# Performance work log

Hardware: AMD Instinct MI355X
Metric: run time of the kernel (lower is better)

Reference implementation:

```python
import math
import jax, jax.numpy as jnp
import numpy as np

D_MODEL = 512
NHEAD = 8
D_HEAD = D_MODEL // NHEAD
TEMP = 0.8
B, LQ, LK = 16, 512, 1024
NEG = -1.0e9


def setup_inputs() -> dict:
    key = jax.random.key(0)
    ks = jax.random.split(key, 12)
    s = 1.0 / math.sqrt(D_MODEL)
    return {
        "Q_src": jax.random.normal(ks[0], (B, LQ, D_MODEL), jnp.float32),
        "KV_src": jax.random.normal(ks[1], (B, LK, D_MODEL), jnp.float32),
        "key_gate": jax.random.uniform(ks[2], (B, LK), jnp.float32, 1e-3, 1.0),
        "key_padding_mask": jax.random.randint(ks[3], (B, LK), 0, 2, jnp.int32),
        "Wq": jax.random.normal(ks[4], (D_MODEL, D_MODEL), jnp.float32) * s,
        "bq": jnp.zeros((D_MODEL,), jnp.float32),
        "Wk": jax.random.normal(ks[5], (D_MODEL, D_MODEL), jnp.float32) * s,
        "bk": jnp.zeros((D_MODEL,), jnp.float32),
        "Wv": jax.random.normal(ks[6], (D_MODEL, D_MODEL), jnp.float32) * s,
        "bv": jnp.zeros((D_MODEL,), jnp.float32),
        "Wo": jax.random.normal(ks[7], (D_MODEL, D_MODEL), jnp.float32) * s,
        "bo": jnp.zeros((D_MODEL,), jnp.float32),
    }


def reference(Q_src, KV_src, key_gate, key_padding_mask, Wq, bq, Wk, bk, Wv, bv, Wo, bo):
    b, lq, _ = Q_src.shape
    lk = KV_src.shape[1]
    # projections -> [B, H, L, Dh]
    q = (Q_src @ Wq + bq).reshape(b, lq, NHEAD, D_HEAD).transpose(0, 2, 1, 3)
    k = (KV_src @ Wk + bk).reshape(b, lk, NHEAD, D_HEAD).transpose(0, 2, 1, 3)
    v = (KV_src @ Wv + bv).reshape(b, lk, NHEAD, D_HEAD).transpose(0, 2, 1, 3)
    # scores with log-gate bias [B, H, Lq, Lk]
    logits = jnp.einsum("bhqd,bhkd->bhqk", q, k) / math.sqrt(D_HEAD)
    logits = logits + jnp.log(key_gate)[:, None, None, :]
    pad = (key_padding_mask == 0)[:, None, None, :]
    logits = jnp.where(pad, NEG, logits) / TEMP
    attn = jax.nn.softmax(logits, axis=-1)
    ctx = jnp.einsum("bhqk,bhkd->bhqd", attn, v)
    ctx = ctx.transpose(0, 2, 1, 3).reshape(b, lq, D_MODEL)
    return ctx @ Wo + bo
```

## Files before the change

kernel.cpp:

```cpp
#include <hip/hip_runtime.h>
#include <math.h>

typedef __bf16 bf16;
typedef __bf16 bf16x8 __attribute__((ext_vector_type(8)));
typedef __bf16 bf16x4 __attribute__((ext_vector_type(4)));
typedef __bf16 bf16x2 __attribute__((ext_vector_type(2)));
typedef float  f32x4  __attribute__((ext_vector_type(4)));
typedef unsigned int uint;

#define SCQ2 0.22542110f
#define SMREF 16.0f

#define VMC(n) asm volatile("s_waitcnt vmcnt(" #n ")" ::: "memory")
#define BARR do { __builtin_amdgcn_s_barrier(); __builtin_amdgcn_sched_barrier(0); } while (0)

#if __has_builtin(__builtin_amdgcn_exp2f)
#define EXP2F __builtin_amdgcn_exp2f
#else
#define EXP2F exp2f
#endif

__device__ __forceinline__ void gload16(const void* g, void* l) {
  __builtin_amdgcn_global_load_lds((const __attribute__((address_space(1))) void*)g,
                                   (__attribute__((address_space(3))) void*)l, 16, 0, 0);
}

__device__ __forceinline__ uint pk2(float a, float b) {
  bf16x2 t = {(bf16)a, (bf16)b};
  return __builtin_bit_cast(uint, t);
}

union V8 { bf16x8 v; bf16x4 h[2]; uint u[4]; };

__global__ void prep_k(const float* __restrict__ Wq, const float* __restrict__ Wk,
                       const float* __restrict__ Wv, const float* __restrict__ Wo,
                       bf16* __restrict__ Tq, bf16* __restrict__ Tkv, bf16* __restrict__ To,
                       const float* __restrict__ gate, const int* __restrict__ mask,
                       float* __restrict__ gfac,
                       const float* __restrict__ Qs, const float* __restrict__ KVs,
                       bf16* __restrict__ Qsb, bf16* __restrict__ KVb) {
  const int bid = blockIdx.x, tid = threadIdx.x;
  if (bid < 256) {
    const int w = bid >> 6, t = bid & 63;
    const float* W = (w == 0) ? Wq : (w == 1) ? Wk : (w == 2) ? Wv : Wo;
    bf16* T = (w == 0) ? Tq : (w == 3) ? To : Tkv;
    const int ro = (w == 2) ? 512 : 0;
    const int k0 = (t >> 3) * 64, n0 = (t & 7) * 64;
    __shared__ bf16 tl[64][72];
#pragma unroll
    for (int i = 0; i < 16; i++) {
      int s = i * 256 + tid;
      int r = s >> 6, c = s & 63;
      tl[r][c] = (bf16)W[(size_t)(k0 + r) * 512 + n0 + c];
    }
    __syncthreads();
#pragma unroll
    for (int i = 0; i < 16; i++) {
      int s = i * 256 + tid;
      int r = s >> 6, c = s & 63;
      T[(size_t)(ro + n0 + r) * 512 + k0 + c] = tl[c][r];
    }
  } else if (bid < 320) {
    int i = (bid - 256) * 256 + tid;
    gfac[i] = mask[i] ? __expf(1.25f * __logf(gate[i])) : 0.0f;
  } else {
    const float* s;
    bf16* d;
    size_t i;
    if (bid < 2368) { s = Qs; d = Qsb; i = ((size_t)(bid - 320) * 256 + tid) * 8; }
    else            { s = KVs; d = KVb; i = ((size_t)(bid - 2368) * 256 + tid) * 8; }
    f32x4 a = *(const f32x4*)(s + i);
    f32x4 b = *(const f32x4*)(s + i + 4);
    bf16x8 o = {(bf16)a[0], (bf16)a[1], (bf16)a[2], (bf16)a[3],
                (bf16)b[0], (bf16)b[1], (bf16)b[2], (bf16)b[3]};
    *(bf16x8*)(d + i) = o;
  }
}

__global__ __launch_bounds__(512, 2) void gemm_kv8(
    const bf16* __restrict__ A, const bf16* __restrict__ Bt,
    const float* __restrict__ kb, const float* __restrict__ vb,
    const float* __restrict__ gfac, bf16* __restrict__ K_out, bf16* __restrict__ V_out) {
  const int tid = threadIdx.x, w = tid >> 6, l = tid & 63;
  const int lg = l >> 4, lr = l & 15;
  const int bid = (int)(blockIdx.x & 7) * 32 + (int)(blockIdx.x >> 3);
  const int bm = (bid >> 2) * 256;
  const int bn = (bid & 3) * 256;
  const int wm = w >> 2, wn = w & 3;

  __shared__ __align__(16) bf16 AB[2][16384];

  const int lrow = l >> 2;
  const int cs = (l & 3) ^ ((l >> 3) & 3);

  f32x4 acc[8][4];
#pragma unroll
  for (int i = 0; i < 8; i++)
#pragma unroll
    for (int j = 0; j < 4; j++) acc[i][j] = (f32x4){0.f, 0.f, 0.f, 0.f};

  auto stA = [&](int p, int u, int kt) {
    const int rb = (w >> 2) * 128 + u * 64 + (w & 3) * 16;
    gload16(A + (size_t)(bm + rb + lrow) * 512 + kt * 32 + cs * 8, &AB[p][rb * 32]);
  };
  auto stB = [&](int p, int u, int kt) {
    const int rb = (w >> 1) * 64 + u * 32 + (w & 1) * 16;
    gload16(Bt + (size_t)(bn + rb + lrow) * 512 + kt * 32 + cs * 8, &AB[p][8192 + rb * 32]);
  };

  bf16x8 aA[4], bb0[2], bb1[2];
#define RDA(p, mh)                                                                   \
  _Pragma("unroll") for (int m2 = 0; m2 < 4; m2++) {                                 \
    const int row = wm * 128 + (mh) * 64 + m2 * 16 + lr;                             \
    aA[m2] = *(const bf16x8*)(&AB[p][row * 32 + ((lg ^ ((row >> 1) & 3)) * 8)]);     \
  }
#define RDB(p, nh, dst)                                                              \
  _Pragma("unroll") for (int n2 = 0; n2 < 2; n2++) {                                 \
    const int row = wn * 64 + (nh) * 32 + n2 * 16 + lr;                              \
    dst[n2] = *(const bf16x8*)(&AB[p][8192 + row * 32 + ((lg ^ ((row >> 1) & 3)) * 8)]); \
  }
#define MM(mh, nh, bbv)                                                              \
  __builtin_amdgcn_s_setprio(1);                                                     \
  _Pragma("unroll") for (int m2 = 0; m2 < 4; m2++)                                   \
  _Pragma("unroll") for (int n2 = 0; n2 < 2; n2++)                                   \
    acc[(mh) * 4 + m2][(nh) * 2 + n2] =                                              \
        __builtin_amdgcn_mfma_f32_16x16x32_bf16(aA[m2], bbv[n2],                     \
                                                acc[(mh) * 4 + m2][(nh) * 2 + n2], 0, 0, 0); \
  __builtin_amdgcn_s_setprio(0);

  stA(0, 0, 0); stB(0, 0, 0); stA(0, 1, 0); stB(0, 1, 0);
  stA(1, 0, 1); stB(1, 0, 1);
  VMC(4);
  BARR;

  for (int i = 0; i < 8; ++i) {
    const bool last = (i == 7);
    const int k1 = 2 * i + 1, k2 = 2 * i + 2, k3 = 2 * i + 3;
    stA(1, 1, k1); stB(1, 1, k1);
    RDA(0, 0); RDB(0, 0, bb0);
    MM(0, 0, bb0);
    VMC(4); BARR;
    RDB(0, 1, bb1);
    MM(0, 1, bb1);
    BARR;
    if (!last) stA(0, 0, k2);
    RDA(0, 1);
    MM(1, 0, bb0);
    BARR;
    if (!last) stB(0, 0, k2);
    MM(1, 1, bb1);
    if (last) { VMC(2); } else { VMC(4); }
    BARR;
    if (!last) { stA(0, 1, k2); stB(0, 1, k2); }
    RDA(1, 0); RDB(1, 0, bb0);
    MM(0, 0, bb0);
    if (last) { VMC(0); } else { VMC(4); }
    BARR;
    RDB(1, 1, bb1);
    MM(0, 1, bb1);
    BARR;
    if (!last) stA(1, 0, k3);
    RDA(1, 1);
    MM(1, 0, bb0);
    BARR;
    if (!last) stB(1, 0, k3);
    MM(1, 1, bb1);
    VMC(4); BARR;
  }
#undef RDA
#undef RDB
#undef MM

  if (bn < 512) {
#pragma unroll
    for (int mf = 0; mf < 8; mf++) {
#pragma unroll
      for (int nf = 0; nf < 4; nf++) {
        f32x4 c = acc[mf][nf];
        const int n = bn + wn * 64 + nf * 16 + lr;
        const int m0 = bm + wm * 128 + mf * 16 + lg * 4;
        const float bias = kb[n];
#pragma unroll
        for (int r = 0; r < 4; r++) K_out[(size_t)(m0 + r) * 512 + n] = (bf16)(c[r] + bias);
      }
    }
  } else {
#pragma unroll
    for (int mf = 0; mf < 8; mf++) {
#pragma unroll
      for (int nf = 0; nf < 4; nf++) {
        f32x4 c = acc[mf][nf];
        const int n = bn + wn * 64 + nf * 16 + lr;
        const int m0 = bm + wm * 128 + mf * 16 + lg * 4;
        const int nn = n - 512;
        const int hh = nn >> 6, dd = nn & 63;
        const int bb = m0 >> 10, key = m0 & 1023;
        const int u = key & 31;
        const int keyp = (key & ~31) + ((u & 15) >> 2) * 8 + ((u >> 4) & 1) * 4;
        const float bias = vb[nn];
        f32x4 g4 = *(const f32x4*)(gfac + m0);
        bf16x4 w4 = {(bf16)((c[0] + bias) * g4[0]), (bf16)((c[1] + bias) * g4[1]),
                     (bf16)((c[2] + bias) * g4[2]), (bf16)((c[3] + bias) * g4[3])};
        *(bf16x4*)(V_out + ((size_t)((bb * 8 + hh) * 64 + dd)) * 1024 + keyp) = w4;
      }
    }
  }
}

template <int OM, int NT, int CHUNK>
__global__ __launch_bounds__(256, 2) void gemm_k(
    const bf16* __restrict__ A, const bf16* __restrict__ Bt,
    const float* __restrict__ b0, void* __restrict__ C0, float scale) {
  const int tid = threadIdx.x, w = tid >> 6, l = tid & 63;
  const int lg = l >> 4, lr = l & 15;
  const int bid = (int)(blockIdx.x & 7) * CHUNK + (int)(blockIdx.x >> 3);
  const int bm = (bid / NT) * 64;
  const int bn = (bid % NT) * 128;
  const int wr = (w >> 1) * 32, wc = (w & 1) * 64;
  __shared__ __align__(16) bf16 As[3][64][32];
  __shared__ __align__(16) bf16 Bs[3][128][32];
  const int r16 = l >> 2;
  const int cs = (l & 3) ^ ((l >> 3) & 3);

  f32x4 acc[2][4];
#pragma unroll
  for (int i = 0; i < 2; i++)
#pragma unroll
    for (int j = 0; j < 4; j++) acc[i][j] = (f32x4){0.f, 0.f, 0.f, 0.f};

  auto stage = [&](int buf, int kt) {
    gload16(A + (size_t)(bm + w * 16 + r16) * 512 + kt * 32 + cs * 8, &As[buf][w * 16][0]);
#pragma unroll
    for (int j = 0; j < 2; j++)
      gload16(Bt + (size_t)(bn + w * 32 + j * 16 + r16) * 512 + kt * 32 + cs * 8,
              &Bs[buf][w * 32 + j * 16][0]);
  };

  stage(0, 0);
  stage(1, 1);
  for (int t = 0; t < 16; ++t) {
    const int buf = t % 3;
    if (t == 15) { VMC(0); } else { VMC(3); }
    BARR;
    if (t < 14) stage((t + 2) % 3, t + 2);
    bf16x8 af[2], bfr[4];
#pragma unroll
    for (int mf = 0; mf < 2; mf++) {
      const int row = wr + mf * 16 + lr;
      af[mf] = *(const bf16x8*)(&As[buf][row][(lg ^ ((row >> 1) & 3)) * 8]);
    }
#pragma unroll
    for (int nf = 0; nf < 4; nf++) {
      const int row = wc + nf * 16 + lr;
      bfr[nf] = *(const bf16x8*)(&Bs[buf][row][(lg ^ ((row >> 1) & 3)) * 8]);
    }
    __builtin_amdgcn_s_setprio(1);
#pragma unroll
    for (int mf = 0; mf < 2; mf++)
#pragma unroll
      for (int nf = 0; nf < 4; nf++)
        acc[mf][nf] = __builtin_amdgcn_mfma_f32_16x16x32_bf16(af[mf], bfr[nf], acc[mf][nf], 0, 0, 0);
    __builtin_amdgcn_s_setprio(0);
  }

#pragma unroll
  for (int mf = 0; mf < 2; mf++) {
#pragma unroll
    for (int nf = 0; nf < 4; nf++) {
      f32x4 c = acc[mf][nf];
      const int n = bn + wc + nf * 16 + lr;
      const int m0 = bm + wr + mf * 16 + lg * 4;
      const float bias = b0[n];
      if constexpr (OM == 0) {
        bf16* C = (bf16*)C0;
#pragma unroll
        for (int r = 0; r < 4; r++) C[(size_t)(m0 + r) * 512 + n] = (bf16)((c[r] + bias) * scale);
      } else {
        float* C = (float*)C0;
#pragma unroll
        for (int r = 0; r < 4; r++) C[(size_t)(m0 + r) * 512 + n] = c[r] + bias;
      }
    }
  }
}

__global__ __launch_bounds__(512, 1) void attn_k(
    const bf16* __restrict__ Q, const bf16* __restrict__ Kb,
    const bf16* __restrict__ Vt, const float* __restrict__ gfac,
    bf16* __restrict__ ctx) {
  const int tid = threadIdx.x, w = tid >> 6, l = tid & 63;
  const int lg = l >> 4, lr = l & 15;
  const int bid = (int)(blockIdx.x & 7) * 32 + (int)(blockIdx.x >> 3);
  const int qb = bid & 1, h = (bid >> 1) & 7, b = bid >> 4;
  const int q0 = qb * 256;

  __shared__ __align__(16) bf16 Ks[2][2][64][64];
  __shared__ __align__(16) bf16 Vs[2][2][64][64];
  __shared__ __align__(16) float gfs[1024];

  bf16x8 qf[2][2];
#pragma unroll
  for (int s = 0; s < 2; s++) {
    const bf16* qp = Q + (size_t)(b * 512 + q0 + w * 32 + s * 16 + lr) * 512 + h * 64;
    qf[s][0] = *(const bf16x8*)(qp + lg * 8);
    qf[s][1] = *(const bf16x8*)(qp + 32 + lg * 8);
  }

  f32x4 o[2][4];
#pragma unroll
  for (int s = 0; s < 2; s++)
#pragma unroll
    for (int i = 0; i < 4; i++) o[s][i] = (f32x4){0.f, 0.f, 0.f, 0.f};
  f32x4 lacc[2] = {(f32x4){0.f, 0.f, 0.f, 0.f}, (f32x4){0.f, 0.f, 0.f, 0.f}};

  const int r8 = l >> 3;
  const int c8g = (l & 7) ^ ((l >> 3) & 7);
  const bf16* Kbase = Kb + ((size_t)b * 1024) * 512 + h * 64 + c8g * 8;
  const bf16* Vbase = Vt + ((size_t)(b * 8 + h) * 64) * 1024 + c8g * 8;

  auto stage = [&](int buf, int t) {
#pragma unroll
    for (int sub = 0; sub < 2; sub++) {
      const int kv0 = t * 128 + sub * 64;
      gload16(Kbase + (size_t)(kv0 + w * 8 + r8) * 512, &Ks[buf][sub][w * 8][0]);
      gload16(Vbase + (size_t)(w * 8 + r8) * 1024 + kv0, &Vs[buf][sub][w * 8][0]);
    }
  };

  if (w < 4) gload16(gfac + b * 1024 + w * 256 + l * 4, &gfs[w * 256]);
  stage(0, 0);
  VMC(0);
  BARR;

  for (int t = 0; t < 8; ++t) {
    const int buf = t & 1;
    if (t < 7) stage(buf ^ 1, t + 1);

#pragma unroll
    for (int sub = 0; sub < 2; sub++) {
      f32x4 gvv[4];
#pragma unroll
      for (int f = 0; f < 4; f++)
        gvv[f] = *(const f32x4*)(&gfs[t * 128 + sub * 64 + f * 16 + lg * 4]);

      f32x4 s4[2][4];
      __builtin_amdgcn_s_setprio(1);
#pragma unroll
      for (int f = 0; f < 4; f++) {
        const int row = f * 16 + lr;
        const bf16x8 k0 = *(const bf16x8*)(&Ks[buf][sub][row][(lg ^ (row & 7)) * 8]);
        const bf16x8 k1 = *(const bf16x8*)(&Ks[buf][sub][row][((4 + lg) ^ (row & 7)) * 8]);
#pragma unroll
        for (int s = 0; s < 2; s++) {
          f32x4 z = (f32x4){-SMREF, -SMREF, -SMREF, -SMREF};
          z = __builtin_amdgcn_mfma_f32_16x16x32_bf16(k0, qf[s][0], z, 0, 0, 0);
          s4[s][f] = __builtin_amdgcn_mfma_f32_16x16x32_bf16(k1, qf[s][1], z, 0, 0, 0);
        }
      }
      __builtin_amdgcn_s_setprio(0);

      V8 pb[2][2];
#pragma unroll
      for (int s = 0; s < 2; s++) {
        float p[4][4];
#pragma unroll
        for (int f = 0; f < 4; f++)
#pragma unroll
          for (int r = 0; r < 4; r++) p[f][r] = EXP2F(s4[s][f][r]);
#pragma unroll
        for (int f = 0; f < 4; f++)
#pragma unroll
          for (int r = 0; r < 4; r++) lacc[s][r] = fmaf(p[f][r], gvv[f][r], lacc[s][r]);
        pb[s][0].u[0] = pk2(p[0][0], p[0][1]); pb[s][0].u[1] = pk2(p[0][2], p[0][3]);
        pb[s][0].u[2] = pk2(p[1][0], p[1][1]); pb[s][0].u[3] = pk2(p[1][2], p[1][3]);
        pb[s][1].u[0] = pk2(p[2][0], p[2][1]); pb[s][1].u[1] = pk2(p[2][2], p[2][3]);
        pb[s][1].u[2] = pk2(p[3][0], p[3][1]); pb[s][1].u[3] = pk2(p[3][2], p[3][3]);
      }

      __builtin_amdgcn_s_setprio(1);
#pragma unroll
      for (int od = 0; od < 4; od++) {
        const int row = od * 16 + lr;
        const bf16x8 va0 = *(const bf16x8*)(&Vs[buf][sub][row][(lg ^ (row & 7)) * 8]);
        const bf16x8 va1 = *(const bf16x8*)(&Vs[buf][sub][row][((4 + lg) ^ (row & 7)) * 8]);
#pragma unroll
        for (int s = 0; s < 2; s++) {
          o[s][od] = __builtin_amdgcn_mfma_f32_16x16x32_bf16(va0, pb[s][0].v, o[s][od], 0, 0, 0);
          o[s][od] = __builtin_amdgcn_mfma_f32_16x16x32_bf16(va1, pb[s][1].v, o[s][od], 0, 0, 0);
        }
      }
      __builtin_amdgcn_s_setprio(0);
    }

    if (t < 7) VMC(0);
    BARR;
  }

#pragma unroll
  for (int s = 0; s < 2; s++) {
    float lp = (lacc[s][0] + lacc[s][1]) + (lacc[s][2] + lacc[s][3]);
    lp += __shfl_xor(lp, 16);
    lp += __shfl_xor(lp, 32);
    const float inv = 1.0f / lp;
    bf16* cp = ctx + (size_t)(b * 512 + q0 + w * 32 + s * 16 + lr) * 512 + h * 64;
#pragma unroll
    for (int od = 0; od < 4; od++)
#pragma unroll
      for (int r = 0; r < 4; r++) cp[od * 16 + lg * 4 + r] = (bf16)(o[s][od][r] * inv);
  }
}

extern "C" void kernel_launch(void* const* d_in, const int* in_sizes, int n_in,
                              void* d_out, int out_size, void* d_ws, size_t ws_size,
                              hipStream_t stream) {
  (void)in_sizes; (void)n_in; (void)out_size; (void)ws_size;
  const float* Q_src = (const float*)d_in[0];
  const float* KV_src = (const float*)d_in[1];
  const float* gate = (const float*)d_in[2];
  const int* mask = (const int*)d_in[3];
  const float* Wq = (const float*)d_in[4];
  const float* bq = (const float*)d_in[5];
  const float* Wk = (const float*)d_in[6];
  const float* bk = (const float*)d_in[7];
  const float* Wv = (const float*)d_in[8];
  const float* bv = (const float*)d_in[9];
  const float* Wo = (const float*)d_in[10];
  const float* bo = (const float*)d_in[11];
  float* out = (float*)d_out;

  char* ws = (char*)d_ws;
  size_t off = 0;
  auto alloc = [&](size_t bytes) {
    char* p = ws + off;
    off += (bytes + 255) & ~(size_t)255;
    return p;
  };
  bf16* Wtq = (bf16*)alloc(512 * 512 * 2);
  bf16* Btkv = (bf16*)alloc(1024 * 512 * 2);
  bf16* Wto = (bf16*)alloc(512 * 512 * 2);
  float* gfac = (float*)alloc(16384 * 4);
  bf16* Qsb = (bf16*)alloc((size_t)8192 * 512 * 2);
  bf16* KVb = (bf16*)alloc((size_t)16384 * 512 * 2);
  bf16* Qb = (bf16*)alloc((size_t)8192 * 512 * 2);
  bf16* Kb = (bf16*)alloc((size_t)16384 * 512 * 2);
  bf16* Vt = (bf16*)alloc((size_t)16384 * 512 * 2);
  bf16* Cx = KVb;

  prep_k<<<6464, 256, 0, stream>>>(Wq, Wk, Wv, Wo, Wtq, Btkv, Wto, gate, mask, gfac,
                                   Q_src, KV_src, Qsb, KVb);
  gemm_kv8<<<256, 512, 0, stream>>>(KVb, Btkv, bk, bv, gfac, Kb, Vt);
  gemm_k<0, 4, 64><<<512, 256, 0, stream>>>(Qsb, Wtq, bq, Qb, SCQ2);
  attn_k<<<256, 512, 0, stream>>>(Qb, Kb, Vt, gfac, Cx);
  gemm_k<2, 4, 64><<<512, 256, 0, stream>>>(Cx, Wto, bo, out, 1.0f);
}
```

Baseline: 84.94 us.

## Split KV range across two wave groups with 64-row Q tiles per wave

Restructures the attention kernel so the 8 waves form two groups that each process half of the key/value sequence, with each wave owning 64 query rows instead of 32. K fragments are loaded from LDS once per tile and reused across four query sub-tiles, which cuts LDS read traffic per MFMA. The two groups' partial outputs and row sums are combined through shared memory at the end. This raises register pressure (twice the accumulators and Q fragments) and adds a final reduction and extra barriers.

After: 86.19 us. No clear change (+1.5%).

```diff
diff --git a/kernel.cpp b/kernel.cpp
--- a/kernel.cpp
+++ b/kernel.cpp
@@ -290,6 +290,7 @@
     bf16* __restrict__ ctx) {
   const int tid = threadIdx.x, w = tid >> 6, l = tid & 63;
   const int lg = l >> 4, lr = l & 15;
+  const int ks = w >> 2, wl = w & 3;
   const int bid = (int)(blockIdx.x & 7) * 32 + (int)(blockIdx.x >> 3);
   const int qb = bid & 1, h = (bid >> 1) & 7, b = bid >> 4;
   const int q0 = qb * 256;
@@ -298,20 +299,21 @@
   __shared__ __align__(16) bf16 Vs[2][2][64][64];
   __shared__ __align__(16) float gfs[1024];
 
-  bf16x8 qf[2][2];
-#pragma unroll
-  for (int s = 0; s < 2; s++) {
-    const bf16* qp = Q + (size_t)(b * 512 + q0 + w * 32 + s * 16 + lr) * 512 + h * 64;
+  bf16x8 qf[4][2];
+#pragma unroll
+  for (int s = 0; s < 4; s++) {
+    const bf16* qp = Q + (size_t)(b * 512 + q0 + wl * 64 + s * 16 + lr) * 512 + h * 64;
     qf[s][0] = *(const bf16x8*)(qp + lg * 8);
     qf[s][1] = *(const bf16x8*)(qp + 32 + lg * 8);
   }
 
-  f32x4 o[2][4];
-#pragma unroll
-  for (int s = 0; s < 2; s++)
+  f32x4 o[4][4];
+#pragma unroll
+  for (int s = 0; s < 4; s++)
 #pragma unroll
     for (int i = 0; i < 4; i++) o[s][i] = (f32x4){0.f, 0.f, 0.f, 0.f};
-  f32x4 lacc[2] = {(f32x4){0.f, 0.f, 0.f, 0.f}, (f32x4){0.f, 0.f, 0.f, 0.f}};
+  f32x4 lacc[4] = {(f32x4){0.f, 0.f, 0.f, 0.f}, (f32x4){0.f, 0.f, 0.f, 0.f},
+                   (f32x4){0.f, 0.f, 0.f, 0.f}, (f32x4){0.f, 0.f, 0.f, 0.f}};
 
   const int r8 = l >> 3;
   const int c8g = (l & 7) ^ ((l >> 3) & 7);
@@ -319,94 +321,119 @@
   const bf16* Vbase = Vt + ((size_t)(b * 8 + h) * 64) * 1024 + c8g * 8;
 
   auto stage = [&](int buf, int t) {
-#pragma unroll
-    for (int sub = 0; sub < 2; sub++) {
-      const int kv0 = t * 128 + sub * 64;
-      gload16(Kbase + (size_t)(kv0 + w * 8 + r8) * 512, &Ks[buf][sub][w * 8][0]);
-      gload16(Vbase + (size_t)(w * 8 + r8) * 1024 + kv0, &Vs[buf][sub][w * 8][0]);
-    }
+    const int kv0 = ks * 512 + t * 64;
+    gload16(Kbase + (size_t)(kv0 + wl * 16 + r8) * 512, &Ks[ks][buf][wl * 16][0]);
+    gload16(Kbase + (size_t)(kv0 + wl * 16 + 8 + r8) * 512, &Ks[ks][buf][wl * 16 + 8][0]);
+    gload16(Vbase + (size_t)(wl * 16 + r8) * 1024 + kv0, &Vs[ks][buf][wl * 16][0]);
+    gload16(Vbase + (size_t)(wl * 16 + 8 + r8) * 1024 + kv0, &Vs[ks][buf][wl * 16 + 8][0]);
   };
 
   if (w < 4) gload16(gfac + b * 1024 + w * 256 + l * 4, &gfs[w * 256]);
   stage(0, 0);
-  VMC(0);
-  BARR;
 
   for (int t = 0; t < 8; ++t) {
     const int buf = t & 1;
+    VMC(0);
+    BARR;
     if (t < 7) stage(buf ^ 1, t + 1);
 
-#pragma unroll
-    for (int sub = 0; sub < 2; sub++) {
-      f32x4 gvv[4];
-#pragma unroll
-      for (int f = 0; f < 4; f++)
-        gvv[f] = *(const f32x4*)(&gfs[t * 128 + sub * 64 + f * 16 + lg * 4]);
-
-      f32x4 s4[2][4];
+    f32x4 gvv[4];
+#pragma unroll
+    for (int f = 0; f < 4; f++)
+      gvv[f] = *(const f32x4*)(&gfs[ks * 512 + t * 64 + f * 16 + lg * 4]);
+
+    bf16x8 kf[4][2];
+#pragma unroll
+    for (int f = 0; f < 4; f++) {
+      const int row = f * 16 + lr;
+      kf[f][0] = *(const bf16x8*)(&Ks[ks][buf][row][(lg ^ (row & 7)) * 8]);
+      kf[f][1] = *(const bf16x8*)(&Ks[ks][buf][row][((4 + lg) ^ (row & 7)) * 8]);
+    }
+
+    V8 pb[4][2];
+#pragma unroll
+    for (int s = 0; s < 4; s++) {
+      f32x4 s4[4];
       __builtin_amdgcn_s_setprio(1);
 #pragma unroll
       for (int f = 0; f < 4; f++) {
-        const int row = f * 16 + lr;
-        const bf16x8 k0 = *(const bf16x8*)(&Ks[buf][sub][row][(lg ^ (row & 7)) * 8]);
-        const bf16x8 k1 = *(const bf16x8*)(&Ks[buf][sub][row][((4 + lg) ^ (row & 7)) * 8]);
-#pragma unroll
-        for (int s = 0; s < 2; s++) {
-          f32x4 z = (f32x4){-SMREF, -SMREF, -SMREF, -SMREF};
-          z = __builtin_amdgcn_mfma_f32_16x16x32_bf16(k0, qf[s][0], z, 0, 0, 0);
-          s4[s][f] = __builtin_amdgcn_mfma_f32_16x16x32_bf16(k1, qf[s][1], z, 0, 0, 0);
-        }
+        f32x4 z = (f32x4){-SMREF, -SMREF, -SMREF, -SMREF};
+        z = __builtin_amdgcn_mfma_f32_16x16x32_bf16(kf[f][0], qf[s][0], z, 0, 0, 0);
+        s4[f] = __builtin_amdgcn_mfma_f32_16x16x32_bf16(kf[f][1], qf[s][1], z, 0, 0, 0);
       }
       __builtin_amdgcn_s_setprio(0);
-
-      V8 pb[2][2];
-#pragma unroll
-      for (int s = 0; s < 2; s++) {
-        float p[4][4];
-#pragma unroll
-        for (int f = 0; f < 4; f++)
-#pragma unroll
-          for (int r = 0; r < 4; r++) p[f][r] = EXP2F(s4[s][f][r]);
-#pragma unroll
-        for (int f = 0; f < 4; f++)
-#pragma unroll
-          for (int r = 0; r < 4; r++) lacc[s][r] = fmaf(p[f][r], gvv[f][r], lacc[s][r]);
-        pb[s][0].u[0] = pk2(p[0][0], p[0][1]); pb[s][0].u[1] = pk2(p[0][2], p[0][3]);
-        pb[s][0].u[2] = pk2(p[1][0], p[1][1]); pb[s][0].u[3] = pk2(p[1][2], p[1][3]);
-        pb[s][1].u[0] = pk2(p[2][0], p[2][1]); pb[s][1].u[1] = pk2(p[2][2], p[2][3]);
-        pb[s][1].u[2] = pk2(p[3][0], p[3][1]); pb[s][1].u[3] = pk2(p[3][2], p[3][3]);
+      float p[4][4];
+#pragma unroll
+      for (int f = 0; f < 4; f++)
+#pragma unroll
+        for (int r = 0; r < 4; r++) p[f][r] = EXP2F(s4[f][r]);
+#pragma unroll
+      for (int f = 0; f < 4; f++)
+#pragma unroll
+        for (int r = 0; r < 4; r++) lacc[s][r] = fmaf(p[f][r], gvv[f][r], lacc[s][r]);
+      pb[s][0].u[0] = pk2(p[0][0], p[0][1]); pb[s][0].u[1] = pk2(p[0][2], p[0][3]);
+      pb[s][0].u[2] = pk2(p[1][0], p[1][1]); pb[s][0].u[3] = pk2(p[1][2], p[1][3]);
+      pb[s][1].u[0] = pk2(p[2][0], p[2][1]); pb[s][1].u[1] = pk2(p[2][2], p[2][3]);
+      pb[s][1].u[2] = pk2(p[3][0], p[3][1]); pb[s][1].u[3] = pk2(p[3][2], p[3][3]);
+    }
+
+    __builtin_amdgcn_s_setprio(1);
+#pragma unroll
+    for (int od = 0; od < 4; od++) {
+      const int row = od * 16 + lr;
+      const bf16x8 va0 = *(const bf16x8*)(&Vs[ks][buf][row][(lg ^ (row & 7)) * 8]);
+      const bf16x8 va1 = *(const bf16x8*)(&Vs[ks][buf][row][((4 + lg) ^ (row & 7)) * 8]);
+#pragma unroll
+      for (int s = 0; s < 4; s++) {
+        o[s][od] = __builtin_amdgcn_mfma_f32_16x16x32_bf16(va0, pb[s][0].v, o[s][od], 0, 0, 0);
+        o[s][od] = __builtin_amdgcn_mfma_f32_16x16x32_bf16(va1, pb[s][1].v, o[s][od], 0, 0, 0);
       }
-
-      __builtin_amdgcn_s_setprio(1);
-#pragma unroll
-      for (int od = 0; od < 4; od++) {
-        const int row = od * 16 + lr;
-        const bf16x8 va0 = *(const bf16x8*)(&Vs[buf][sub][row][(lg ^ (row & 7)) * 8]);
-        const bf16x8 va1 = *(const bf16x8*)(&Vs[buf][sub][row][((4 + lg) ^ (row & 7)) * 8]);
-#pragma unroll
-        for (int s = 0; s < 2; s++) {
-          o[s][od] = __builtin_amdgcn_mfma_f32_16x16x32_bf16(va0, pb[s][0].v, o[s][od], 0, 0, 0);
-          o[s][od] = __builtin_amdgcn_mfma_f32_16x16x32_bf16(va1, pb[s][1].v, o[s][od], 0, 0, 0);
-        }
-      }
-      __builtin_amdgcn_s_setprio(0);
-    }
-
-    if (t < 7) VMC(0);
-    BARR;
-  }
-
-#pragma unroll
-  for (int s = 0; s < 2; s++) {
-    float lp = (lacc[s][0] + lacc[s][1]) + (lacc[s][2] + lacc[s][3]);
-    lp += __shfl_xor(lp, 16);
-    lp += __shfl_xor(lp, 32);
-    const float inv = 1.0f / lp;
-    bf16* cp = ctx + (size_t)(b * 512 + q0 + w * 32 + s * 16 + lr) * 512 + h * 64;
-#pragma unroll
-    for (int od = 0; od < 4; od++)
-#pragma unroll
-      for (int r = 0; r < 4; r++) cp[od * 16 + lg * 4 + r] = (bf16)(o[s][od][r] * inv);
+    }
+    __builtin_amdgcn_s_setprio(0);
+  }
+
+  f32x4* OmA = (f32x4*)&Ks[0][0][0][0];
+  f32x4* OmB = (f32x4*)&Vs[0][0][0][0];
+  float* Lp = (float*)gfs;
+  __syncthreads();
+  if (ks == 1) {
+    const int base = (wl * 64 + l) * 8;
+#pragma unroll
+    for (int s = 0; s < 2; s++)
+#pragma unroll
+      for (int od = 0; od < 4; od++) OmA[base + ((s * 4 + od) ^ (l & 7))] = o[s][od];
+#pragma unroll
+    for (int s = 2; s < 4; s++)
+#pragma unroll
+      for (int od = 0; od < 4; od++) OmB[base + (((s - 2) * 4 + od) ^ (l & 7))] = o[s][od];
+#pragma unroll
+    for (int s = 0; s < 4; s++)
+      Lp[(wl * 64 + l) * 4 + s] = (lacc[s][0] + lacc[s][1]) + (lacc[s][2] + lacc[s][3]);
+  }
+  __syncthreads();
+  if (ks == 0) {
+    const int base = (wl * 64 + l) * 8;
+#pragma unroll
+    for (int s = 0; s < 2; s++)
+#pragma unroll
+      for (int od = 0; od < 4; od++) o[s][od] += OmA[base + ((s * 4 + od) ^ (l & 7))];
+#pragma unroll
+    for (int s = 2; s < 4; s++)
+#pragma unroll
+      for (int od = 0; od < 4; od++) o[s][od] += OmB[base + (((s - 2) * 4 + od) ^ (l & 7))];
+#pragma unroll
+    for (int s = 0; s < 4; s++) {
+      float lp = (lacc[s][0] + lacc[s][1]) + (lacc[s][2] + lacc[s][3]) +
+                 Lp[(wl * 64 + l) * 4 + s];
+      lp += __shfl_xor(lp, 16);
+      lp += __shfl_xor(lp, 32);
+      const float inv = 1.0f / lp;
+      bf16* cp = ctx + (size_t)(b * 512 + q0 + wl * 64 + s * 16 + lr) * 512 + h * 64;
+#pragma unroll
+      for (int od = 0; od < 4; od++)
+#pragma unroll
+        for (int r = 0; r < 4; r++) cp[od * 16 + lg * 4 + r] = (bf16)(o[s][od][r] * inv);
+    }
   }
 }
 
```
